# Kernel optimization log

Measured on AMD Instinct MI355X. Metric: run time of the kernel, lower is better.

The kernel has to match this reference:

```python
import jax, jax.numpy as jnp
import numpy as np


def setup_inputs() -> dict:
    key = jax.random.key(0)
    k0, k1, k2, k3, k4, k5 = jax.random.split(key, 6)
    B, V, Fin, K, Fout = 8, 49152, 64, 3, 64
    nnz = V * 8  # ~8 neighbors per vertex (HEALPix sphere graph)
    std = (2.0 / (Fin * K)) ** 0.5  # Kaiming-normal as in reset_parameters
    inputs = jax.random.normal(k0, (B, V, Fin), jnp.float32)
    weight = jax.random.normal(k1, (Fin, K, Fout), jnp.float32) * std
    bias = jax.random.normal(k2, (Fout,), jnp.float32) * 0.05
    lap_rows = jax.random.randint(k3, (nnz,), 0, V, jnp.int32)
    lap_cols = jax.random.randint(k4, (nnz,), 0, V, jnp.int32)
    lap_vals = jax.random.normal(k5, (nnz,), jnp.float32) * 0.1
    return {"inputs": inputs, "weight": weight, "bias": bias,
            "lap_rows": lap_rows, "lap_cols": lap_cols, "lap_vals": lap_vals}


def reference(inputs, weight, bias, lap_rows, lap_cols, lap_vals):
    B, V, Fin = inputs.shape
    _, K, Fout = weight.shape

    def spmm(x):  # sparse Laplacian (COO) @ dense [V, Fin*B]
        return jax.ops.segment_sum(lap_vals[:, None] * x[lap_cols], lap_rows,
                                   num_segments=V)

    # x0: [V, Fin*B], matching torch's permute(1,2,0).view(V, Fin*B)
    x0 = inputs.transpose(1, 2, 0).reshape(V, Fin * B)
    xs = [x0]
    if K > 1:
        x1 = spmm(x0)
        xs.append(x1)
    for _ in range(2, K):
        x2 = 2.0 * spmm(x1) - x0  # Chebyshev recurrence
        xs.append(x2)
        x0, x1 = x1, x2
    x = jnp.stack(xs)                                    # [K, V, Fin*B]
    x = x.reshape(K, V, Fin, B).transpose(3, 1, 2, 0)    # [B, V, Fin, K]
    x = x.reshape(B * V, Fin * K)
    out = x @ weight.reshape(Fin * K, Fout)              # dense GEMM
    return out.reshape(B, V, Fout) + bias
```

## Files before the change

### kernel.cpp

```cpp
#include <hip/hip_runtime.h>
#include <stdint.h>

#define B_   8
#define V_   49152
#define M_   (B_ * V_)
#define CAP_ 48

typedef unsigned short ushort_t;
typedef __attribute__((ext_vector_type(8))) short short8;
typedef __attribute__((ext_vector_type(4))) float float4v;

__device__ __forceinline__ float bf2f_lo(unsigned int pk) {
    union { unsigned int u; float f; } x; x.u = pk << 16; return x.f;
}
__device__ __forceinline__ float bf2f_hi(unsigned int pk) {
    union { unsigned int u; float f; } x; x.u = pk & 0xffff0000u; return x.f;
}
__device__ __forceinline__ ushort_t f2bf(float f) {
    union { unsigned int u; float f; } x; x.f = f;
    unsigned int u = x.u;
    unsigned int r = u + 0x7fffu + ((u >> 16) & 1u);
    return (ushort_t)(r >> 16);
}
__device__ __forceinline__ unsigned int pack2(float a, float b) {
    return ((unsigned int)f2bf(b) << 16) | (unsigned int)f2bf(a);
}
__device__ __forceinline__ void fma8(float* acc, float w, const uint4& p) {
    const unsigned int* u = (const unsigned int*)&p;
    #pragma unroll
    for (int i = 0; i < 4; i++) {
        acc[2 * i]     += w * bf2f_lo(u[i]);
        acc[2 * i + 1] += w * bf2f_hi(u[i]);
    }
}

__global__ void fill_sentinel(float* out, int n) {
    int i = blockIdx.x * blockDim.x + threadIdx.x;
    if (i < n) out[i] = 9999.0f;
}

#define PREP_B 3072
__global__ __launch_bounds__(256) void k1_fused(const float* __restrict__ inp,
                                                ushort_t* __restrict__ x0t,
                                                const int* __restrict__ rows,
                                                const int* __restrict__ cols,
                                                const float* __restrict__ vals, int nnz,
                                                int* __restrict__ cursor,
                                                uint2* __restrict__ e_cv,
                                                const float* __restrict__ wgt,
                                                ushort_t* __restrict__ wBf) {
    int bid = blockIdx.x;
    int t = threadIdx.x;
    if (bid < PREP_B) {
        int idx = bid * 256 + t;
        int f4 = idx & 15, v = idx >> 4;
        #pragma unroll
        for (int b = 0; b < 8; b++) {
            float4 d = *(const float4*)(inp + ((size_t)b * V_ + v) * 64 + f4 * 4);
            uint2 o = make_uint2(pack2(d.x, d.y), pack2(d.z, d.w));
            *(uint2*)(x0t + ((size_t)v * 8 + b) * 64 + f4 * 4) = o;
        }
    } else if (bid < PREP_B + 48) {
        int idx = (bid - PREP_B) * 256 + t;
        int j = idx & 7, lane = (idx >> 3) & 63, ntc = (idx >> 9) & 3, kb = idx >> 11;
        int k = kb * 32 + (lane >> 4) * 8 + j;
        int kc = k >> 6, fi = k & 63;
        int fo = ntc * 16 + (lane & 15);
        float w;
        if (kc == 0)      w = wgt[(fi * 3 + 0) * 64 + fo] - wgt[(fi * 3 + 2) * 64 + fo];
        else if (kc == 1) w = wgt[(fi * 3 + 1) * 64 + fo];
        else              w = 2.0f * wgt[(fi * 3 + 2) * 64 + fo];
        wBf[idx] = f2bf(w);
    } else {
        int i = (bid - PREP_B - 48) * 256 + t;
        if (i < nnz) {
            int r = rows[i];
            int pos = atomicAdd(&cursor[r], 1);
            if (pos < CAP_)
                e_cv[(size_t)r * CAP_ + pos] = make_uint2((unsigned int)cols[i],
                                                          __float_as_uint(vals[i]));
        }
    }
}

__device__ __forceinline__ void gather16(const ushort_t* __restrict__ srcbf,
                                         const uint2* __restrict__ e_cv,
                                         int beg, int end, float* acc) {
    for (int e = beg; e < end; e += 8) {
        uint4 E0 = *(const uint4*)(e_cv + e);
        uint4 E1 = *(const uint4*)(e_cv + e + 2);
        uint4 E2 = *(const uint4*)(e_cv + e + 4);
        uint4 E3 = *(const uint4*)(e_cv + e + 6);
        const ushort_t* p0 = srcbf + ((size_t)E0.x * 512);
        const ushort_t* p1 = srcbf + ((size_t)E0.z * 512);
        const ushort_t* p2 = srcbf + ((size_t)E1.x * 512);
        const ushort_t* p3 = srcbf + ((size_t)E1.z * 512);
        const ushort_t* p4 = srcbf + ((size_t)E2.x * 512);
        const ushort_t* p5 = srcbf + ((size_t)E2.z * 512);
        const ushort_t* p6 = srcbf + ((size_t)E3.x * 512);
        const ushort_t* p7 = srcbf + ((size_t)E3.z * 512);
        uint4 a0 = *(const uint4*)p0, b0 = *(const uint4*)(p0 + 8);
        uint4 a1 = *(const uint4*)p1, b1 = *(const uint4*)(p1 + 8);
        uint4 a2 = *(const uint4*)p2, b2 = *(const uint4*)(p2 + 8);
        uint4 a3 = *(const uint4*)p3, b3 = *(const uint4*)(p3 + 8);
        uint4 a4 = *(const uint4*)p4, b4 = *(const uint4*)(p4 + 8);
        uint4 a5 = *(const uint4*)p5, b5 = *(const uint4*)(p5 + 8);
        uint4 a6 = *(const uint4*)p6, b6 = *(const uint4*)(p6 + 8);
        uint4 a7 = *(const uint4*)p7, b7 = *(const uint4*)(p7 + 8);
        float w0 = __uint_as_float(E0.y), w1 = __uint_as_float(E0.w);
        float w2 = __uint_as_float(E1.y), w3 = __uint_as_float(E1.w);
        float w4 = __uint_as_float(E2.y), w5 = __uint_as_float(E2.w);
        float w6 = __uint_as_float(E3.y), w7 = __uint_as_float(E3.w);
        fma8(acc, w0, a0); fma8(acc + 8, w0, b0);
        fma8(acc, w1, a1); fma8(acc + 8, w1, b1);
        fma8(acc, w2, a2); fma8(acc + 8, w2, b2);
        fma8(acc, w3, a3); fma8(acc + 8, w3, b3);
        fma8(acc, w4, a4); fma8(acc + 8, w4, b4);
        fma8(acc, w5, a5); fma8(acc + 8, w5, b5);
        fma8(acc, w6, a6); fma8(acc + 8, w6, b6);
        fma8(acc, w7, a7); fma8(acc + 8, w7, b7);
    }
}

__global__ __launch_bounds__(256) void spmm1_kernel(const ushort_t* __restrict__ x0t,
                                                    const int* __restrict__ cursor,
                                                    const uint2* __restrict__ e_cv,
                                                    ushort_t* __restrict__ x1) {
    int t = threadIdx.x;
    int vi = t >> 5, b = (t >> 2) & 7, f8 = t & 3;
    int v = blockIdx.x * 8 + vi;
    int beg = v * CAP_;
    int end = beg + ((cursor[v] + 7) & ~7);
    float acc[16];
    #pragma unroll
    for (int i = 0; i < 16; i++) acc[i] = 0.f;
    gather16(x0t + b * 64 + f8 * 16, e_cv, beg, end, acc);
    unsigned int opk[8];
    #pragma unroll
    for (int i = 0; i < 8; i++) opk[i] = pack2(acc[2 * i], acc[2 * i + 1]);
    ushort_t* dst = x1 + ((size_t)v * 8 + b) * 64 + f8 * 16;
    *(uint4*)dst       = make_uint4(opk[0], opk[1], opk[2], opk[3]);
    *(uint4*)(dst + 8) = make_uint4(opk[4], opk[5], opk[6], opk[7]);
}

__global__ __launch_bounds__(256) void spmm2_gemm(const ushort_t* __restrict__ x0t,
                                                  const ushort_t* __restrict__ x1,
                                                  const int* __restrict__ cursor,
                                                  const uint2* __restrict__ e_cv,
                                                  const ushort_t* __restrict__ wBf,
                                                  const float* __restrict__ bias,
                                                  float* __restrict__ out) {
    __shared__ ushort_t sh[64 * 72];
    int t = threadIdx.x;
    int lane = t & 63, wv = t >> 6;
    int quad = lane >> 4, col = lane & 15;
    int v0 = blockIdx.x * 8;
    int m0 = v0 * 8 + wv * 16;

    size_t arow = (size_t)(m0 + col) * 64 + quad * 8;
    short8 A0[2], A1[2];
    A0[0] = *(const short8*)(x0t + arow);
    A0[1] = *(const short8*)(x0t + arow + 32);
    A1[0] = *(const short8*)(x1 + arow);
    A1[1] = *(const short8*)(x1 + arow + 32);

    int vi = t >> 5, b = (t >> 2) & 7, f8 = t & 3;
    int v = v0 + vi;
    int beg = v * CAP_;
    int end = beg + ((cursor[v] + 7) & ~7);
    float acc[16];
    #pragma unroll
    for (int i = 0; i < 16; i++) acc[i] = 0.f;
    gather16(x1 + b * 64 + f8 * 16, e_cv, beg, end, acc);

    unsigned int opk[8];
    #pragma unroll
    for (int i = 0; i < 8; i++) opk[i] = pack2(acc[2 * i], acc[2 * i + 1]);
    int mg = vi * 8 + b;
    ushort_t* dst = sh + mg * 72 + f8 * 16;
    *(uint4*)dst       = make_uint4(opk[0], opk[1], opk[2], opk[3]);
    *(uint4*)(dst + 8) = make_uint4(opk[4], opk[5], opk[6], opk[7]);
    __syncthreads();

    short8 Bf[6][4];
    #pragma unroll
    for (int kb = 0; kb < 6; kb++)
        #pragma unroll
        for (int ntc = 0; ntc < 4; ntc++)
            Bf[kb][ntc] = *(const short8*)(wBf + ((size_t)((kb * 4 + ntc) * 64 + lane)) * 8);

    float bv[4];
    #pragma unroll
    for (int ntc = 0; ntc < 4; ntc++) bv[ntc] = bias[ntc * 16 + col];

    float4v accm[4];
    #pragma unroll
    for (int ntc = 0; ntc < 4; ntc++) accm[ntc] = (float4v){0.f, 0.f, 0.f, 0.f};

    #pragma unroll
    for (int p = 0; p < 2; p++) {
        #pragma unroll
        for (int ntc = 0; ntc < 4; ntc++)
            accm[ntc] = __builtin_amdgcn_mfma_f32_16x16x32_bf16(A0[p], Bf[p][ntc], accm[ntc], 0, 0, 0);
    }
    #pragma unroll
    for (int p = 0; p < 2; p++) {
        #pragma unroll
        for (int ntc = 0; ntc < 4; ntc++)
            accm[ntc] = __builtin_amdgcn_mfma_f32_16x16x32_bf16(A1[p], Bf[2 + p][ntc], accm[ntc], 0, 0, 0);
    }
    #pragma unroll
    for (int p = 0; p < 2; p++) {
        short8 A = *(const short8*)(sh + (wv * 16 + col) * 72 + quad * 8 + p * 32);
        #pragma unroll
        for (int ntc = 0; ntc < 4; ntc++)
            accm[ntc] = __builtin_amdgcn_mfma_f32_16x16x32_bf16(A, Bf[4 + p][ntc], accm[ntc], 0, 0, 0);
    }

    #pragma unroll
    for (int reg = 0; reg < 4; reg++) {
        int m = m0 + quad * 4 + reg;
        int vv = m >> 3, bb = m & 7;
        float* orow = out + ((size_t)bb * V_ + vv) * 64;
        #pragma unroll
        for (int ntc = 0; ntc < 4; ntc++)
            orow[ntc * 16 + col] = accm[ntc][reg] + bv[ntc];
    }
}

extern "C" void kernel_launch(void* const* d_in, const int* in_sizes, int n_in,
                              void* d_out, int out_size, void* d_ws, size_t ws_size,
                              hipStream_t stream) {
    const float* inp  = (const float*)d_in[0];
    const float* wgt  = (const float*)d_in[1];
    const float* bias = (const float*)d_in[2];
    const int*   rows = (const int*)d_in[3];
    const int*   cols = (const int*)d_in[4];
    const float* vals = (const float*)d_in[5];
    int nnz = in_sizes[3];
    float* out = (float*)d_out;
    (void)n_in; (void)out_size;

    char* ws = (char*)d_ws;
    size_t o = 0;
    auto alloc = [&](size_t bytes) { void* p = ws + o; o += (bytes + 255) & ~(size_t)255; return p; };
    size_t meta0 = o;
    int*      cursor = (int*)alloc((size_t)V_ * 4);
    uint2*    e_cv   = (uint2*)alloc((size_t)V_ * CAP_ * 8);
    size_t meta_bytes = o - meta0;
    ushort_t* x0t    = (ushort_t*)alloc((size_t)M_ * 64 * 2);
    ushort_t* x1     = (ushort_t*)alloc((size_t)M_ * 64 * 2);
    ushort_t* wBf    = (ushort_t*)alloc(6 * 4 * 64 * 8 * 2);

    if (ws_size < o) {
        fill_sentinel<<<(M_ * 64 + 255) / 256, 256, 0, stream>>>(out, M_ * 64);
        return;
    }

    int hb = (nnz + 255) / 256;
    hipMemsetAsync((char*)ws + meta0, 0, meta_bytes, stream);
    k1_fused<<<PREP_B + 48 + hb, 256, 0, stream>>>(inp, x0t, rows, cols, vals, nnz,
                                                   cursor, e_cv, wgt, wBf);
    spmm1_kernel<<<V_ / 8, 256, 0, stream>>>(x0t, cursor, e_cv, x1);
    spmm2_gemm<<<V_ / 8, 256, 0, stream>>>(x0t, x1, cursor, e_cv, wBf, bias, out);
}
```

Baseline: 352.1 us.

## Fuse memset and three stages into one cooperative persistent kernel with grid syncs

Replaces the memset plus three separate kernel launches with a single cooperative persistent kernel. It zeroes the metadata, runs the prep, SpMM1 and SpMM2+GEMM stages in grid-stride loops, and separates them with grid.sync(). The gather loop is also changed to process 4 edges per iteration instead of 8, with row ends padded to 4 and clamped to CAP. This removes launch gaps and tail effects between stages, but adds grid-wide barrier costs. It also caps the grid at 2048 blocks and gives up some memory-level parallelism per gather iteration.

After: 1.000 ms. 184% more time.

```diff
diff --git a/kernel.cpp b/kernel.cpp
--- a/kernel.cpp
+++ b/kernel.cpp
@@ -1,10 +1,14 @@
 #include <hip/hip_runtime.h>
+#include <hip/hip_cooperative_groups.h>
 #include <stdint.h>
+
+namespace cg = cooperative_groups;
 
 #define B_   8
 #define V_   49152
 #define M_   (B_ * V_)
 #define CAP_ 48
+#define PREP_B 3072
 
 typedef unsigned short ushort_t;
 typedef __attribute__((ext_vector_type(8))) short short8;
@@ -39,20 +43,18 @@
     if (i < n) out[i] = 9999.0f;
 }
 
-#define PREP_B 3072
-__global__ __launch_bounds__(256) void k1_fused(const float* __restrict__ inp,
-                                                ushort_t* __restrict__ x0t,
-                                                const int* __restrict__ rows,
-                                                const int* __restrict__ cols,
-                                                const float* __restrict__ vals, int nnz,
-                                                int* __restrict__ cursor,
-                                                uint2* __restrict__ e_cv,
-                                                const float* __restrict__ wgt,
-                                                ushort_t* __restrict__ wBf) {
-    int bid = blockIdx.x;
-    int t = threadIdx.x;
-    if (bid < PREP_B) {
-        int idx = bid * 256 + t;
+__device__ __forceinline__ void k1_unit(int u, int t,
+                                        const float* __restrict__ inp,
+                                        ushort_t* __restrict__ x0t,
+                                        const int* __restrict__ rows,
+                                        const int* __restrict__ cols,
+                                        const float* __restrict__ vals, int nnz,
+                                        int* __restrict__ cursor,
+                                        uint2* __restrict__ e_cv,
+                                        const float* __restrict__ wgt,
+                                        ushort_t* __restrict__ wBf) {
+    if (u < PREP_B) {
+        int idx = u * 256 + t;
         int f4 = idx & 15, v = idx >> 4;
         #pragma unroll
         for (int b = 0; b < 8; b++) {
@@ -60,8 +62,8 @@
             uint2 o = make_uint2(pack2(d.x, d.y), pack2(d.z, d.w));
             *(uint2*)(x0t + ((size_t)v * 8 + b) * 64 + f4 * 4) = o;
         }
-    } else if (bid < PREP_B + 48) {
-        int idx = (bid - PREP_B) * 256 + t;
+    } else if (u < PREP_B + 48) {
+        int idx = (u - PREP_B) * 256 + t;
         int j = idx & 7, lane = (idx >> 3) & 63, ntc = (idx >> 9) & 3, kb = idx >> 11;
         int k = kb * 32 + (lane >> 4) * 8 + j;
         int kc = k >> 6, fi = k & 63;
@@ -72,7 +74,7 @@
         else              w = 2.0f * wgt[(fi * 3 + 2) * 64 + fo];
         wBf[idx] = f2bf(w);
     } else {
-        int i = (bid - PREP_B - 48) * 256 + t;
+        int i = (u - PREP_B - 48) * 256 + t;
         if (i < nnz) {
             int r = rows[i];
             int pos = atomicAdd(&cursor[r], 1);
@@ -86,61 +88,152 @@
 __device__ __forceinline__ void gather16(const ushort_t* __restrict__ srcbf,
                                          const uint2* __restrict__ e_cv,
                                          int beg, int end, float* acc) {
-    for (int e = beg; e < end; e += 8) {
+    for (int e = beg; e < end; e += 4) {
         uint4 E0 = *(const uint4*)(e_cv + e);
         uint4 E1 = *(const uint4*)(e_cv + e + 2);
-        uint4 E2 = *(const uint4*)(e_cv + e + 4);
-        uint4 E3 = *(const uint4*)(e_cv + e + 6);
+        float w0 = __uint_as_float(E0.y), w1 = __uint_as_float(E0.w);
+        float w2 = __uint_as_float(E1.y), w3 = __uint_as_float(E1.w);
         const ushort_t* p0 = srcbf + ((size_t)E0.x * 512);
         const ushort_t* p1 = srcbf + ((size_t)E0.z * 512);
         const ushort_t* p2 = srcbf + ((size_t)E1.x * 512);
         const ushort_t* p3 = srcbf + ((size_t)E1.z * 512);
-        const ushort_t* p4 = srcbf + ((size_t)E2.x * 512);
-        const ushort_t* p5 = srcbf + ((size_t)E2.z * 512);
-        const ushort_t* p6 = srcbf + ((size_t)E3.x * 512);
-        const ushort_t* p7 = srcbf + ((size_t)E3.z * 512);
         uint4 a0 = *(const uint4*)p0, b0 = *(const uint4*)(p0 + 8);
         uint4 a1 = *(const uint4*)p1, b1 = *(const uint4*)(p1 + 8);
         uint4 a2 = *(const uint4*)p2, b2 = *(const uint4*)(p2 + 8);
         uint4 a3 = *(const uint4*)p3, b3 = *(const uint4*)(p3 + 8);
-        uint4 a4 = *(const uint4*)p4, b4 = *(const uint4*)(p4 + 8);
-        uint4 a5 = *(const uint4*)p5, b5 = *(const uint4*)(p5 + 8);
-        uint4 a6 = *(const uint4*)p6, b6 = *(const uint4*)(p6 + 8);
-        uint4 a7 = *(const uint4*)p7, b7 = *(const uint4*)(p7 + 8);
-        float w0 = __uint_as_float(E0.y), w1 = __uint_as_float(E0.w);
-        float w2 = __uint_as_float(E1.y), w3 = __uint_as_float(E1.w);
-        float w4 = __uint_as_float(E2.y), w5 = __uint_as_float(E2.w);
-        float w6 = __uint_as_float(E3.y), w7 = __uint_as_float(E3.w);
         fma8(acc, w0, a0); fma8(acc + 8, w0, b0);
         fma8(acc, w1, a1); fma8(acc + 8, w1, b1);
         fma8(acc, w2, a2); fma8(acc + 8, w2, b2);
         fma8(acc, w3, a3); fma8(acc + 8, w3, b3);
-        fma8(acc, w4, a4); fma8(acc + 8, w4, b4);
-        fma8(acc, w5, a5); fma8(acc + 8, w5, b5);
-        fma8(acc, w6, a6); fma8(acc + 8, w6, b6);
-        fma8(acc, w7, a7); fma8(acc + 8, w7, b7);
-    }
+    }
+}
+
+__device__ __forceinline__ int row_end(const int* cursor, int v) {
+    int c = cursor[v];
+    if (c > CAP_) c = CAP_;
+    return v * CAP_ + ((c + 3) & ~3);
+}
+
+__device__ __forceinline__ void spmm1_unit(int u, int t,
+                                           const ushort_t* __restrict__ x0t,
+                                           const int* __restrict__ cursor,
+                                           const uint2* __restrict__ e_cv,
+                                           ushort_t* __restrict__ x1) {
+    int vi = t >> 5, b = (t >> 2) & 7, f8 = t & 3;
+    int v = u * 8 + vi;
+    float acc[16];
+    #pragma unroll
+    for (int i = 0; i < 16; i++) acc[i] = 0.f;
+    gather16(x0t + b * 64 + f8 * 16, e_cv, v * CAP_, row_end(cursor, v), acc);
+    unsigned int opk[8];
+    #pragma unroll
+    for (int i = 0; i < 8; i++) opk[i] = pack2(acc[2 * i], acc[2 * i + 1]);
+    ushort_t* dst = x1 + ((size_t)v * 8 + b) * 64 + f8 * 16;
+    *(uint4*)dst       = make_uint4(opk[0], opk[1], opk[2], opk[3]);
+    *(uint4*)(dst + 8) = make_uint4(opk[4], opk[5], opk[6], opk[7]);
+}
+
+__device__ __forceinline__ void spmm2_unit(int u, int t,
+                                           const ushort_t* __restrict__ x0t,
+                                           const ushort_t* __restrict__ x1,
+                                           const int* __restrict__ cursor,
+                                           const uint2* __restrict__ e_cv,
+                                           const ushort_t* __restrict__ wBf,
+                                           const float* __restrict__ bias,
+                                           float* __restrict__ out) {
+    __shared__ ushort_t sh[64 * 72];
+    int lane = t & 63, wv = t >> 6;
+    int quad = lane >> 4, col = lane & 15;
+    int v0 = u * 8;
+    int m0 = v0 * 8 + wv * 16;
+
+    size_t arow = (size_t)(m0 + col) * 64 + quad * 8;
+    short8 A0[2], A1[2];
+    A0[0] = *(const short8*)(x0t + arow);
+    A0[1] = *(const short8*)(x0t + arow + 32);
+    A1[0] = *(const short8*)(x1 + arow);
+    A1[1] = *(const short8*)(x1 + arow + 32);
+
+    int vi = t >> 5, b = (t >> 2) & 7, f8 = t & 3;
+    int v = v0 + vi;
+    float acc[16];
+    #pragma unroll
+    for (int i = 0; i < 16; i++) acc[i] = 0.f;
+    gather16(x1 + b * 64 + f8 * 16, e_cv, v * CAP_, row_end(cursor, v), acc);
+
+    unsigned int opk[8];
+    #pragma unroll
+    for (int i = 0; i < 8; i++) opk[i] = pack2(acc[2 * i], acc[2 * i + 1]);
+    int mg = vi * 8 + b;
+    ushort_t* dst = sh + mg * 72 + f8 * 16;
+    *(uint4*)dst       = make_uint4(opk[0], opk[1], opk[2], opk[3]);
+    *(uint4*)(dst + 8) = make_uint4(opk[4], opk[5], opk[6], opk[7]);
+    __syncthreads();
+
+    short8 Bf[6][4];
+    #pragma unroll
+    for (int kb = 0; kb < 6; kb++)
+        #pragma unroll
+        for (int ntc = 0; ntc < 4; ntc++)
+            Bf[kb][ntc] = *(const short8*)(wBf + ((size_t)((kb * 4 + ntc) * 64 + lane)) * 8);
+
+    float bv[4];
+    #pragma unroll
+    for (int ntc = 0; ntc < 4; ntc++) bv[ntc] = bias[ntc * 16 + col];
+
+    float4v accm[4];
+    #pragma unroll
+    for (int ntc = 0; ntc < 4; ntc++) accm[ntc] = (float4v){0.f, 0.f, 0.f, 0.f};
+
+    #pragma unroll
+    for (int p = 0; p < 2; p++) {
+        #pragma unroll
+        for (int ntc = 0; ntc < 4; ntc++)
+            accm[ntc] = __builtin_amdgcn_mfma_f32_16x16x32_bf16(A0[p], Bf[p][ntc], accm[ntc], 0, 0, 0);
+    }
+    #pragma unroll
+    for (int p = 0; p < 2; p++) {
+        #pragma unroll
+        for (int ntc = 0; ntc < 4; ntc++)
+            accm[ntc] = __builtin_amdgcn_mfma_f32_16x16x32_bf16(A1[p], Bf[2 + p][ntc], accm[ntc], 0, 0, 0);
+    }
+    #pragma unroll
+    for (int p = 0; p < 2; p++) {
+        short8 A = *(const short8*)(sh + (wv * 16 + col) * 72 + quad * 8 + p * 32);
+        #pragma unroll
+        for (int ntc = 0; ntc < 4; ntc++)
+            accm[ntc] = __builtin_amdgcn_mfma_f32_16x16x32_bf16(A, Bf[4 + p][ntc], accm[ntc], 0, 0, 0);
+    }
+
+    #pragma unroll
+    for (int reg = 0; reg < 4; reg++) {
+        int m = m0 + quad * 4 + reg;
+        int vv = m >> 3, bb = m & 7;
+        float* orow = out + ((size_t)bb * V_ + vv) * 64;
+        #pragma unroll
+        for (int ntc = 0; ntc < 4; ntc++)
+            orow[ntc * 16 + col] = accm[ntc][reg] + bv[ntc];
+    }
+    __syncthreads();
+}
+
+__global__ __launch_bounds__(256) void k1_fused(const float* __restrict__ inp,
+                                                ushort_t* __restrict__ x0t,
+                                                const int* __restrict__ rows,
+                                                const int* __restrict__ cols,
+                                                const float* __restrict__ vals, int nnz,
+                                                int* __restrict__ cursor,
+                                                uint2* __restrict__ e_cv,
+                                                const float* __restrict__ wgt,
+                                                ushort_t* __restrict__ wBf) {
+    k1_unit(blockIdx.x, threadIdx.x, inp, x0t, rows, cols, vals, nnz, cursor, e_cv, wgt, wBf);
 }
 
 __global__ __launch_bounds__(256) void spmm1_kernel(const ushort_t* __restrict__ x0t,
                                                     const int* __restrict__ cursor,
                                                     const uint2* __restrict__ e_cv,
                                                     ushort_t* __restrict__ x1) {
-    int t = threadIdx.x;
-    int vi = t >> 5, b = (t >> 2) & 7, f8 = t & 3;
-    int v = blockIdx.x * 8 + vi;
-    int beg = v * CAP_;
-    int end = beg + ((cursor[v] + 7) & ~7);
-    float acc[16];
-    #pragma unroll
-    for (int i = 0; i < 16; i++) acc[i] = 0.f;
-    gather16(x0t + b * 64 + f8 * 16, e_cv, beg, end, acc);
-    unsigned int opk[8];
-    #pragma unroll
-    for (int i = 0; i < 8; i++) opk[i] = pack2(acc[2 * i], acc[2 * i + 1]);
-    ushort_t* dst = x1 + ((size_t)v * 8 + b) * 64 + f8 * 16;
-    *(uint4*)dst       = make_uint4(opk[0], opk[1], opk[2], opk[3]);
-    *(uint4*)(dst + 8) = make_uint4(opk[4], opk[5], opk[6], opk[7]);
+    spmm1_unit(blockIdx.x, threadIdx.x, x0t, cursor, e_cv, x1);
 }
 
 __global__ __launch_bounds__(256) void spmm2_gemm(const ushort_t* __restrict__ x0t,
@@ -150,82 +243,35 @@
                                                   const ushort_t* __restrict__ wBf,
                                                   const float* __restrict__ bias,
                                                   float* __restrict__ out) {
-    __shared__ ushort_t sh[64 * 72];
+    spmm2_unit(blockIdx.x, threadIdx.x, x0t, x1, cursor, e_cv, wBf, bias, out);
+}
+
+struct KArgs {
+    const float* inp; const float* wgt; const float* bias;
+    const int* rows; const int* cols; const float* vals;
+    int nnz; int hb;
+    int* cursor; uint2* e_cv;
+    ushort_t* x0t; ushort_t* x1; ushort_t* wBf;
+    float* out;
+    uint4* zbase; long long z16;
+};
+
+__global__ __launch_bounds__(256, 8) void mega_kernel(KArgs a) {
+    cg::grid_group grid = cg::this_grid();
     int t = threadIdx.x;
-    int lane = t & 63, wv = t >> 6;
-    int quad = lane >> 4, col = lane & 15;
-    int v0 = blockIdx.x * 8;
-    int m0 = v0 * 8 + wv * 16;
-
-    size_t arow = (size_t)(m0 + col) * 64 + quad * 8;
-    short8 A0[2], A1[2];
-    A0[0] = *(const short8*)(x0t + arow);
-    A0[1] = *(const short8*)(x0t + arow + 32);
-    A1[0] = *(const short8*)(x1 + arow);
-    A1[1] = *(const short8*)(x1 + arow + 32);
-
-    int vi = t >> 5, b = (t >> 2) & 7, f8 = t & 3;
-    int v = v0 + vi;
-    int beg = v * CAP_;
-    int end = beg + ((cursor[v] + 7) & ~7);
-    float acc[16];
-    #pragma unroll
-    for (int i = 0; i < 16; i++) acc[i] = 0.f;
-    gather16(x1 + b * 64 + f8 * 16, e_cv, beg, end, acc);
-
-    unsigned int opk[8];
-    #pragma unroll
-    for (int i = 0; i < 8; i++) opk[i] = pack2(acc[2 * i], acc[2 * i + 1]);
-    int mg = vi * 8 + b;
-    ushort_t* dst = sh + mg * 72 + f8 * 16;
-    *(uint4*)dst       = make_uint4(opk[0], opk[1], opk[2], opk[3]);
-    *(uint4*)(dst + 8) = make_uint4(opk[4], opk[5], opk[6], opk[7]);
-    __syncthreads();
-
-    short8 Bf[6][4];
-    #pragma unroll
-    for (int kb = 0; kb < 6; kb++)
-        #pragma unroll
-        for (int ntc = 0; ntc < 4; ntc++)
-            Bf[kb][ntc] = *(const short8*)(wBf + ((size_t)((kb * 4 + ntc) * 64 + lane)) * 8);
-
-    float bv[4];
-    #pragma unroll
-    for (int ntc = 0; ntc < 4; ntc++) bv[ntc] = bias[ntc * 16 + col];
-
-    float4v accm[4];
-    #pragma unroll
-    for (int ntc = 0; ntc < 4; ntc++) accm[ntc] = (float4v){0.f, 0.f, 0.f, 0.f};
-
-    #pragma unroll
-    for (int p = 0; p < 2; p++) {
-        #pragma unroll
-        for (int ntc = 0; ntc < 4; ntc++)
-            accm[ntc] = __builtin_amdgcn_mfma_f32_16x16x32_bf16(A0[p], Bf[p][ntc], accm[ntc], 0, 0, 0);
-    }
-    #pragma unroll
-    for (int p = 0; p < 2; p++) {
-        #pragma unroll
-        for (int ntc = 0; ntc < 4; ntc++)
-            accm[ntc] = __builtin_amdgcn_mfma_f32_16x16x32_bf16(A1[p], Bf[2 + p][ntc], accm[ntc], 0, 0, 0);
-    }
-    #pragma unroll
-    for (int p = 0; p < 2; p++) {
-        short8 A = *(const short8*)(sh + (wv * 16 + col) * 72 + quad * 8 + p * 32);
-        #pragma unroll
-        for (int ntc = 0; ntc < 4; ntc++)
-            accm[ntc] = __builtin_amdgcn_mfma_f32_16x16x32_bf16(A, Bf[4 + p][ntc], accm[ntc], 0, 0, 0);
-    }
-
-    #pragma unroll
-    for (int reg = 0; reg < 4; reg++) {
-        int m = m0 + quad * 4 + reg;
-        int vv = m >> 3, bb = m & 7;
-        float* orow = out + ((size_t)bb * V_ + vv) * 64;
-        #pragma unroll
-        for (int ntc = 0; ntc < 4; ntc++)
-            orow[ntc * 16 + col] = accm[ntc][reg] + bv[ntc];
-    }
+    int G = gridDim.x;
+    for (long long i = (long long)blockIdx.x * 256 + t; i < a.z16; i += (long long)G * 256)
+        a.zbase[i] = make_uint4(0u, 0u, 0u, 0u);
+    grid.sync();
+    int n1 = PREP_B + 48 + a.hb;
+    for (int u = blockIdx.x; u < n1; u += G)
+        k1_unit(u, t, a.inp, a.x0t, a.rows, a.cols, a.vals, a.nnz, a.cursor, a.e_cv, a.wgt, a.wBf);
+    grid.sync();
+    for (int u = blockIdx.x; u < V_ / 8; u += G)
+        spmm1_unit(u, t, a.x0t, a.cursor, a.e_cv, a.x1);
+    grid.sync();
+    for (int u = blockIdx.x; u < V_ / 8; u += G)
+        spmm2_unit(u, t, a.x0t, a.x1, a.cursor, a.e_cv, a.wBf, a.bias, a.out);
 }
 
 extern "C" void kernel_launch(void* const* d_in, const int* in_sizes, int n_in,
@@ -258,9 +304,36 @@
     }
 
     int hb = (nnz + 255) / 256;
-    hipMemsetAsync((char*)ws + meta0, 0, meta_bytes, stream);
-    k1_fused<<<PREP_B + 48 + hb, 256, 0, stream>>>(inp, x0t, rows, cols, vals, nnz,
-                                                   cursor, e_cv, wgt, wBf);
-    spmm1_kernel<<<V_ / 8, 256, 0, stream>>>(x0t, cursor, e_cv, x1);
-    spmm2_gemm<<<V_ / 8, 256, 0, stream>>>(x0t, x1, cursor, e_cv, wBf, bias, out);
-}
+
+    static int maxBlkPerCU = -2;
+    if (maxBlkPerCU == -2) {
+        int mb = 0;
+        hipError_t e = hipOccupancyMaxActiveBlocksPerMultiprocessor(&mb, mega_kernel, 256, 0);
+        maxBlkPerCU = (e == hipSuccess && mb > 0) ? mb : 0;
+    }
+    bool done = false;
+    if (maxBlkPerCU > 0) {
+        int G = maxBlkPerCU * 256;
+        if (G > 2048) G = 2048;
+        KArgs a;
+        a.inp = inp; a.wgt = wgt; a.bias = bias;
+        a.rows = rows; a.cols = cols; a.vals = vals;
+        a.nnz = nnz; a.hb = hb;
+        a.cursor = cursor; a.e_cv = e_cv;
+        a.x0t = x0t; a.x1 = x1; a.wBf = wBf;
+        a.out = out;
+        a.zbase = (uint4*)(ws + meta0);
+        a.z16 = (long long)(meta_bytes / 16);
+        void* kargs[] = { &a };
+        hipError_t e = hipLaunchCooperativeKernel((const void*)mega_kernel,
+                                                  dim3(G), dim3(256), kargs, 0, stream);
+        done = (e == hipSuccess);
+    }
+    if (!done) {
+        hipMemsetAsync((char*)ws + meta0, 0, meta_bytes, stream);
+        k1_fused<<<PREP_B + 48 + hb, 256, 0, stream>>>(inp, x0t, rows, cols, vals, nnz,
+                                                       cursor, e_cv, wgt, wBf);
+        spmm1_kernel<<<V_ / 8, 256, 0, stream>>>(x0t, cursor, e_cv, x1);
+        spmm2_gemm<<<V_ / 8, 256, 0, stream>>>(x0t, x1, cursor, e_cv, wBf, bias, out);
+    }
+}
```
